# Optimization experiments

Measured on AMD Instinct MI355X. Metric: run time of the kernel, lower is better.

Reference implementation:

```python
import jax, jax.numpy as jnp
import numpy as np

EPS = 1e-6  # matches the ~1e-6 diagonal jitter added in tensor_log


def _make_spd(key, shape_bm, d):
    a = jax.random.normal(key, shape_bm + (d, d), dtype=jnp.float32)
    x = jnp.einsum('bmik,bmjk->bmij', a, a) / d
    return x + 0.1 * jnp.eye(d, dtype=jnp.float32)


def _make_stiefel(key, out_dim, in_dim):
    a = jax.random.normal(key, (in_dim, out_dim), dtype=jnp.float32)
    q, _ = jnp.linalg.qr(a)  # (in_dim, out_dim), orthonormal columns
    return q.T  # (out_dim, in_dim), semi-orthogonal rows


def setup_inputs() -> dict:
    key = jax.random.key(0)
    ks = jax.random.split(key, 8)
    bs, m, din, dqk, dv = 32, 64, 96, 48, 48
    return {
        'x1': _make_spd(ks[0], (bs, m), din),
        'x2': _make_spd(ks[1], (bs, m), din),
        'wq1': _make_stiefel(ks[2], dqk, din),
        'wk1': _make_stiefel(ks[3], dqk, din),
        'wv1': _make_stiefel(ks[4], dv, din),
        'wq2': _make_stiefel(ks[5], dqk, din),
        'wk2': _make_stiefel(ks[6], dqk, din),
        'wv2': _make_stiefel(ks[7], dv, din),
    }


def _logm(t):
    # symmetric matrix log via eigh (inputs SPD); tiny diag jitter as in torch tensor_log
    d = t.shape[-1]
    t = t + EPS * jnp.eye(d, dtype=t.dtype)
    s, u = jnp.linalg.eigh(t)
    return jnp.einsum('...ik,...k,...jk->...ij', u, jnp.log(s), u)


def _expm(t):
    s, u = jnp.linalg.eigh(t)
    return jnp.einsum('...ik,...k,...jk->...ij', u, jnp.exp(s), u)


def _bimap(x, w):
    # SPDTransform: W X W^T, W: (out, in), x: [..., in, in]
    return jnp.einsum('oi,...ij,pj->...op', w, x, w)


def reference(x1, x2, wq1, wk1, wv1, wq2, wk2, wv2):
    # per-stream q/k/v BiMap transforms, then concat along token axis
    Q = jnp.concatenate([_bimap(x1, wq1), _bimap(x2, wq2)], axis=1)  # [b, m, dqk, dqk]
    K = jnp.concatenate([_bimap(x1, wk1), _bimap(x2, wk2)], axis=1)
    V = jnp.concatenate([_bimap(x1, wv1), _bimap(x2, wv2)], axis=1)  # [b, m, dv, dv]

    logQ, logK, logV = _logm(Q), _logm(K), _logm(V)

    # log-Euclidean distance: sum of singular values of D D^T = ||D||_F^2,
    # D = logQ_j - logK_i. energy[b, i, j] matches torch repeat/expand layout
    q2 = jnp.sum(logQ * logQ, axis=(-2, -1))  # [b, m]
    k2 = jnp.sum(logK * logK, axis=(-2, -1))  # [b, m]
    cross = jnp.einsum('bjxy,bixy->bij', logQ, logK)  # [b, i(K), j(Q)]
    energy = q2[:, None, :] + k2[:, :, None] - 2.0 * cross
    energy = jnp.maximum(energy, 0.0)

    scores = 1.0 / (1.0 + jnp.log1p(energy))
    prob = jax.nn.softmax(scores, axis=-2)  # softmax over K index
    prob = jnp.transpose(prob, (0, 2, 1))   # [b, j, i]

    bs, m, dv, _ = V.shape
    mixed = (prob @ logV.reshape(bs, m, dv * dv)).reshape(bs, m, dv, dv)
    out = _expm(mixed)
    out = out[:, -1:, :, :]  # keep_only_last=True
    return out.reshape(-1, dv, dv)  # [bs, dv, dv]
```

## Files before the change

### kernel.cpp

```cpp
#include <hip/hip_runtime.h>
#include <math.h>

#define D_CHEB 24

typedef __attribute__((ext_vector_type(8))) short bf16x8;
typedef __attribute__((ext_vector_type(4))) float f32x4;
typedef __attribute__((ext_vector_type(4))) unsigned int u32x4;

struct Cheb {
    float c[D_CHEB + 1];
    float sm;
    float sbd;
};

__device__ __forceinline__ void split8(const f32x4 a, const f32x4 b,
                                       bf16x8& hi, bf16x8& lo)
{
    float v[8] = {a[0], a[1], a[2], a[3], b[0], b[1], b[2], b[3]};
    unsigned h16[8], l16[8];
    #pragma unroll
    for (int j = 0; j < 8; ++j) {
        unsigned u = __float_as_uint(v[j]);
        unsigned r = (u + 0x7FFFu + ((u >> 16) & 1u)) >> 16;
        h16[j] = r;
        float res = v[j] - __uint_as_float(r << 16);
        l16[j] = __float_as_uint(res) >> 16;
    }
    unsigned hw[4], lw[4];
    #pragma unroll
    for (int q = 0; q < 4; ++q) {
        hw[q] = h16[2 * q] | (h16[2 * q + 1] << 16);
        lw[q] = l16[2 * q] | (l16[2 * q + 1] << 16);
    }
    hi = __builtin_bit_cast(bf16x8, (u32x4){hw[0], hw[1], hw[2], hw[3]});
    lo = __builtin_bit_cast(bf16x8, (u32x4){lw[0], lw[1], lw[2], lw[3]});
}

__global__ __launch_bounds__(256) void split_w(
    const float* __restrict__ w0, const float* __restrict__ w1,
    const float* __restrict__ w2, const float* __restrict__ w3,
    const float* __restrict__ w4,
    unsigned short* __restrict__ whi, unsigned short* __restrict__ wlo)
{
    const float* W = (blockIdx.x == 0) ? w0 : (blockIdx.x == 1) ? w1
                   : (blockIdx.x == 2) ? w2 : (blockIdx.x == 3) ? w3 : w4;
    const int base = blockIdx.x * 4608;
    for (int e = threadIdx.x; e < 4608; e += 256) {
        float f = W[e];
        unsigned u = __float_as_uint(f);
        unsigned r = (u + 0x7FFFu + ((u >> 16) & 1u)) >> 16;
        whi[base + e] = (unsigned short)r;
        float res = f - __uint_as_float(r << 16);
        wlo[base + e] = (unsigned short)(__float_as_uint(res) >> 16);
    }
}

#define TLP 104
__global__ __launch_bounds__(64, 3) void bimap_kernel(
    const float* __restrict__ x1, const float* __restrict__ x2,
    const unsigned short* __restrict__ whi,
    const unsigned short* __restrict__ wlo,
    float* __restrict__ mats)
{
    __shared__ float Tlds[48 * TLP];
    const int bid = blockIdx.x, l = threadIdx.x;
    const int lc = l & 15, lg = l >> 4;

    const float* x; int wi[2]; size_t oo[2]; int npass;
    if (bid < 4096) {
        int b = bid >> 7, s = (bid >> 6) & 1, m = bid & 63;
        x = (s ? x2 : x1) + (size_t)(b * 64 + m) * 9216;
        wi[0] = s ? 2 : 0;
        wi[1] = s ? 3 : 1;
        oo[0] = (size_t)bid; oo[1] = (size_t)(4096 + bid); npass = 2;
    } else {
        int b = bid - 4096;
        x = x2 + (size_t)(b * 64 + 63) * 9216;
        wi[0] = 4; wi[1] = 4;
        oo[0] = (size_t)(8192 + b); oo[1] = oo[0]; npass = 1;
    }

    for (int pass = 0; pass < npass; ++pass) {
        const unsigned short* Wh = whi + wi[pass] * 4608;
        const unsigned short* Wl = wlo + wi[pass] * 4608;

        f32x4 C[3][6];
        #pragma unroll
        for (int tr = 0; tr < 3; ++tr)
            #pragma unroll
            for (int tc = 0; tc < 6; ++tc)
                C[tr][tc] = (f32x4){0.f, 0.f, 0.f, 0.f};
        #pragma unroll
        for (int kb = 0; kb < 3; ++kb) {
            bf16x8 ah[3], al[3];
            #pragma unroll
            for (int tr = 0; tr < 3; ++tr) {
                const int off = (16 * tr + lc) * 96 + kb * 32 + lg * 8;
                ah[tr] = *(const bf16x8*)(Wh + off);
                al[tr] = *(const bf16x8*)(Wl + off);
            }
            #pragma unroll
            for (int tc = 0; tc < 6; ++tc) {
                const float* xp = x + (16 * tc + lc) * 96 + kb * 32 + lg * 8;
                bf16x8 bh, bl;
                split8(*(const f32x4*)xp, *(const f32x4*)(xp + 4), bh, bl);
                #pragma unroll
                for (int tr = 0; tr < 3; ++tr) {
                    C[tr][tc] = __builtin_amdgcn_mfma_f32_16x16x32_bf16(ah[tr], bh, C[tr][tc], 0, 0, 0);
                    C[tr][tc] = __builtin_amdgcn_mfma_f32_16x16x32_bf16(ah[tr], bl, C[tr][tc], 0, 0, 0);
                    C[tr][tc] = __builtin_amdgcn_mfma_f32_16x16x32_bf16(al[tr], bh, C[tr][tc], 0, 0, 0);
                }
            }
        }
        #pragma unroll
        for (int tr = 0; tr < 3; ++tr)
            #pragma unroll
            for (int tc = 0; tc < 6; ++tc)
                #pragma unroll
                for (int q = 0; q < 4; ++q)
                    Tlds[(16 * tr + 4 * lg + q) * TLP + 16 * tc + lc] = C[tr][tc][q];

        f32x4 D[3][3];
        #pragma unroll
        for (int tr = 0; tr < 3; ++tr)
            #pragma unroll
            for (int tc = 0; tc < 3; ++tc)
                D[tr][tc] = (f32x4){0.f, 0.f, 0.f, 0.f};
        #pragma unroll
        for (int kb = 0; kb < 3; ++kb) {
            bf16x8 ah[3], al[3];
            #pragma unroll
            for (int tr = 0; tr < 3; ++tr) {
                const float* tp = &Tlds[(16 * tr + lc) * TLP + kb * 32 + lg * 8];
                split8(*(const f32x4*)tp, *(const f32x4*)(tp + 4), ah[tr], al[tr]);
            }
            #pragma unroll
            for (int tc = 0; tc < 3; ++tc) {
                const int off = (16 * tc + lc) * 96 + kb * 32 + lg * 8;
                bf16x8 bh = *(const bf16x8*)(Wh + off);
                bf16x8 bl = *(const bf16x8*)(Wl + off);
                #pragma unroll
                for (int tr = 0; tr < 3; ++tr) {
                    D[tr][tc] = __builtin_amdgcn_mfma_f32_16x16x32_bf16(ah[tr], bh, D[tr][tc], 0, 0, 0);
                    D[tr][tc] = __builtin_amdgcn_mfma_f32_16x16x32_bf16(ah[tr], bl, D[tr][tc], 0, 0, 0);
                    D[tr][tc] = __builtin_amdgcn_mfma_f32_16x16x32_bf16(al[tr], bh, D[tr][tc], 0, 0, 0);
                }
            }
        }
        float* out = mats + oo[pass] * 2304;
        #pragma unroll
        for (int tr = 0; tr < 3; ++tr)
            #pragma unroll
            for (int tc = 0; tc < 3; ++tc)
                #pragma unroll
                for (int q = 0; q < 4; ++q)
                    out[(16 * tr + 4 * lg + q) * 48 + 16 * tc + lc] = D[tr][tc][q];
    }
}

__global__ __launch_bounds__(64, 3) void logm_kernel(float* __restrict__ mats, Cheb co)
{
    __shared__ __align__(16) unsigned short Ybuf[2 * 48 * 64];
    char* ldsb = (char*)Ybuf;
    const int l = threadIdx.x;
    const int lc = l & 15, lg = l >> 4;
    const int rloc = lg * 4;
    float* A = mats + (size_t)blockIdx.x * 2304;

    bf16x8 Ah[3][2], Al[3][2];
    const float cD = co.c[D_CHEB], cD1 = co.c[D_CHEB - 1];
    #pragma unroll
    for (int tr = 0; tr < 3; ++tr) {
        #pragma unroll
        for (int kb = 0; kb < 2; ++kb) {
            const int row = 16 * tr + lc;
            const int k0 = kb * 32 + lg * 8;
            unsigned shw[4] = {0,0,0,0}, slw[4] = {0,0,0,0};
            unsigned yhw[4] = {0,0,0,0}, ylw[4] = {0,0,0,0};
            if (k0 < 48) {
                const float* ap = A + row * 48 + k0;
                f32x4 a0 = *(const f32x4*)ap;
                f32x4 a1 = *(const f32x4*)(ap + 4);
                float av[8] = {a0[0],a0[1],a0[2],a0[3],a1[0],a1[1],a1[2],a1[3]};
                unsigned sh[8], sl[8], yh[8], yl[8];
                #pragma unroll
                for (int j = 0; j < 8; ++j) {
                    const bool diag = (row == k0 + j);
                    float s = co.sm * av[j] + (diag ? co.sbd : 0.f);
                    float y = cD * s + (diag ? cD1 : 0.f);
                    unsigned us = __float_as_uint(s);
                    sh[j] = us >> 16;
                    sl[j] = __float_as_uint(s - __uint_as_float(us & 0xFFFF0000u)) >> 16;
                    unsigned uy = __float_as_uint(y);
                    yh[j] = uy >> 16;
                    yl[j] = __float_as_uint(y - __uint_as_float(uy & 0xFFFF0000u)) >> 16;
                }
                #pragma unroll
                for (int q = 0; q < 4; ++q) {
                    shw[q] = sh[2*q] | (sh[2*q+1] << 16);
                    slw[q] = sl[2*q] | (sl[2*q+1] << 16);
                    yhw[q] = yh[2*q] | (yh[2*q+1] << 16);
                    ylw[q] = yl[2*q] | (yl[2*q+1] << 16);
                }
            }
            Ah[tr][kb] = __builtin_bit_cast(bf16x8, (u32x4){shw[0],shw[1],shw[2],shw[3]});
            Al[tr][kb] = __builtin_bit_cast(bf16x8, (u32x4){slw[0],slw[1],slw[2],slw[3]});
            const int soff = row * 128 + ((2 * k0) ^ ((row & 7) << 4));
            *(u32x4*)(ldsb + soff)        = (u32x4){yhw[0],yhw[1],yhw[2],yhw[3]};
            *(u32x4*)(ldsb + 6144 + soff) = (u32x4){ylw[0],ylw[1],ylw[2],ylw[3]};
        }
    }

    f32x4 Ya[9], Yb[9];
    #pragma unroll
    for (int t = 0; t < 9; ++t) {
        const int tr = t / 3, tc = t % 3;
        #pragma unroll
        for (int q = 0; q < 4; ++q) {
            const int row = 16 * tr + rloc + q, col = 16 * tc + lc;
            const bool diag = (row == col);
            float a = A[row * 48 + col];
            float s = co.sm * a + (diag ? co.sbd : 0.f);
            Ya[t][q] = cD * s + (diag ? cD1 : 0.f);
            Yb[t][q] = diag ? cD : 0.f;
        }
    }

    int boff[3][2];
    #pragma unroll
    for (int tc = 0; tc < 3; ++tc)
        #pragma unroll
        for (int kb = 0; kb < 2; ++kb) {
            const int row = 16 * tc + lc;
            boff[tc][kb] = row * 128 + ((kb * 64 + lg * 16) ^ ((row & 7) << 4));
        }
    int woff[3][4];
    #pragma unroll
    for (int tc = 0; tc < 3; ++tc)
        #pragma unroll
        for (int q = 0; q < 4; ++q) {
            const int rq = rloc + q;
            woff[tc][q] = rq * 128 + ((32 * tc + 2 * lc) ^ ((rq & 7) << 4));
        }

    auto MM = [&](f32x4 (&T)[9]) {
        #pragma unroll
        for (int tc = 0; tc < 3; ++tc) {
            #pragma unroll
            for (int kb = 0; kb < 2; ++kb) {
                bf16x8 bh = *(const bf16x8*)(ldsb + boff[tc][kb]);
                bf16x8 bl = *(const bf16x8*)(ldsb + 6144 + boff[tc][kb]);
                #pragma unroll
                for (int tr = 0; tr < 3; ++tr) {
                    T[tr*3+tc] = __builtin_amdgcn_mfma_f32_16x16x32_bf16(Ah[tr][kb], bh, T[tr*3+tc], 0, 0, 0);
                    T[tr*3+tc] = __builtin_amdgcn_mfma_f32_16x16x32_bf16(Ah[tr][kb], bl, T[tr*3+tc], 0, 0, 0);
                    T[tr*3+tc] = __builtin_amdgcn_mfma_f32_16x16x32_bf16(Al[tr][kb], bh, T[tr*3+tc], 0, 0, 0);
                }
            }
        }
    };
    auto SPLITW = [&](f32x4 (&T)[9]) {
        #pragma unroll
        for (int t = 0; t < 9; ++t) {
            const int tr = t / 3, tc = t % 3;
            #pragma unroll
            for (int q = 0; q < 4; ++q) {
                float v = T[t][q];
                unsigned u = __float_as_uint(v);
                unsigned lo = __float_as_uint(v - __uint_as_float(u & 0xFFFF0000u)) >> 16;
                const int off = tr * 2048 + woff[tc][q];
                *(unsigned short*)(ldsb + off) = (unsigned short)(u >> 16);
                *(unsigned short*)(ldsb + 6144 + off) = (unsigned short)lo;
            }
        }
    };
    auto INITK = [&](f32x4 (&T)[9], float ck) {
        #pragma unroll
        for (int t = 0; t < 9; ++t) {
            const int tr = t / 3, tc = t % 3;
            #pragma unroll
            for (int q = 0; q < 4; ++q) {
                const float d = (tr == tc && rloc + q == lc) ? ck : 0.f;
                T[t][q] = d - T[t][q];
            }
        }
    };

    for (int k = D_CHEB - 2; k >= 2; k -= 2) {
        INITK(Yb, co.c[k]);     MM(Yb);  SPLITW(Yb);
        INITK(Ya, co.c[k - 1]); MM(Ya);  SPLITW(Ya);
    }
    #pragma unroll
    for (int t = 0; t < 9; ++t) {
        const int tr = t / 3, tc = t % 3;
        #pragma unroll
        for (int q = 0; q < 4; ++q) {
            const float d = (tr == tc && rloc + q == lc) ? co.c[0] : 0.f;
            Yb[t][q] = d - 2.f * Yb[t][q];
        }
    }
    MM(Yb);
    #pragma unroll
    for (int t = 0; t < 9; ++t) {
        const int tr = t / 3, tc = t % 3;
        #pragma unroll
        for (int q = 0; q < 4; ++q)
            A[(16 * tr + rloc + q) * 48 + 16 * tc + lc] = Yb[t][q];
    }
}

__global__ __launch_bounds__(64) void energy_kernel(const float* __restrict__ mats,
                                                    float* __restrict__ sc)
{
    const int i = blockIdx.x, b = blockIdx.y, lane = threadIdx.x;
    const float* K = mats + (size_t)(b * 128 + i) * 2304;
    const float* Q = mats + (size_t)(8192 + b) * 2304;
    float p = 0.f;
    #pragma unroll
    for (int j = 0; j < 9; ++j) {
        int f = (lane + 64 * j) * 4;
        float4 kv = *(const float4*)(K + f);
        float4 qv = *(const float4*)(Q + f);
        float dx = kv.x - qv.x, dy = kv.y - qv.y, dz = kv.z - qv.z, dw = kv.w - qv.w;
        p += dx * dx + dy * dy + dz * dz + dw * dw;
    }
    #pragma unroll
    for (int off = 32; off >= 1; off >>= 1) p += __shfl_xor(p, off, 64);
    if (lane == 0)
        sc[b * 128 + i] = 1.f / (1.f + log1pf(fmaxf(p, 0.f)));
}

__global__ __launch_bounds__(64) void softmax_kernel(float* __restrict__ sc)
{
    const int b = blockIdx.x, lane = threadIdx.x;
    float s0 = sc[b * 128 + lane], s1 = sc[b * 128 + 64 + lane];
    float m = fmaxf(s0, s1);
    #pragma unroll
    for (int off = 32; off >= 1; off >>= 1) m = fmaxf(m, __shfl_xor(m, off, 64));
    float e0 = expf(s0 - m), e1 = expf(s1 - m);
    float sum = e0 + e1;
    #pragma unroll
    for (int off = 32; off >= 1; off >>= 1) sum += __shfl_xor(sum, off, 64);
    sc[b * 128 + lane] = e0 / sum;
    sc[b * 128 + 64 + lane] = e1 / sum;
}

__global__ __launch_bounds__(256) void mix_kernel(const float* __restrict__ mats,
                                                  const float* __restrict__ sc,
                                                  float* __restrict__ mixed)
{
    __shared__ float w[128];
    const int b = blockIdx.y, g = blockIdx.x, tid = threadIdx.x;
    if (tid < 128) w[tid] = sc[b * 128 + tid];
    __syncthreads();
    const int e = g * 256 + tid;
    float acc = 0.f;
    for (int i = 0; i < 128; ++i)
        acc += w[i] * mats[(size_t)(4096 + b * 128 + i) * 2304 + e];
    mixed[(size_t)b * 2304 + e] = acc;
}

__global__ __launch_bounds__(256) void expm_kernel(const float* __restrict__ mixed,
                                                   float* __restrict__ out)
{
    __shared__ float Bs[48][49];
    __shared__ float Ra[48][49];
    __shared__ float Rb[48][49];
    const int b = blockIdx.x, tid = threadIdx.x;
    const float* M = mixed + (size_t)b * 2304;
    for (int e = tid; e < 2304; e += 256) {
        int r = e / 48, c = e % 48;
        float v = 0.25f * M[e];
        Bs[r][c] = v;
        Ra[r][c] = ((r == c) ? 1.f : 0.f) + v * (1.f / 12.f);
    }
    __syncthreads();
    const int tr = tid >> 4, tc = tid & 15;
    const int r0 = tr * 3, c0 = tc * 3;
    float* cur = &Ra[0][0];
    float* nxt = &Rb[0][0];
    for (int k = 11; k >= 1; --k) {
        const float invk = 1.f / (float)k;
        float acc[3][3];
        #pragma unroll
        for (int i = 0; i < 3; ++i)
            #pragma unroll
            for (int j = 0; j < 3; ++j) acc[i][j] = 0.f;
        #pragma unroll 4
        for (int kk = 0; kk < 48; ++kk) {
            float a0 = Bs[r0][kk], a1 = Bs[r0 + 1][kk], a2 = Bs[r0 + 2][kk];
            float b0 = cur[kk * 49 + c0], b1 = cur[kk * 49 + c0 + 1], b2 = cur[kk * 49 + c0 + 2];
            acc[0][0] += a0 * b0; acc[0][1] += a0 * b1; acc[0][2] += a0 * b2;
            acc[1][0] += a1 * b0; acc[1][1] += a1 * b1; acc[1][2] += a1 * b2;
            acc[2][0] += a2 * b0; acc[2][1] += a2 * b1; acc[2][2] += a2 * b2;
        }
        #pragma unroll
        for (int i = 0; i < 3; ++i)
            #pragma unroll
            for (int j = 0; j < 3; ++j)
                nxt[(r0 + i) * 49 + (c0 + j)] =
                    ((r0 + i) == (c0 + j) ? 1.f : 0.f) + acc[i][j] * invk;
        __syncthreads();
        float* t = cur; cur = nxt; nxt = t;
    }
    for (int sq = 0; sq < 2; ++sq) {
        float acc[3][3];
        #pragma unroll
        for (int i = 0; i < 3; ++i)
            #pragma unroll
            for (int j = 0; j < 3; ++j) acc[i][j] = 0.f;
        #pragma unroll 4
        for (int kk = 0; kk < 48; ++kk) {
            float a0 = cur[(r0) * 49 + kk], a1 = cur[(r0 + 1) * 49 + kk], a2 = cur[(r0 + 2) * 49 + kk];
            float b0 = cur[kk * 49 + c0], b1 = cur[kk * 49 + c0 + 1], b2 = cur[kk * 49 + c0 + 2];
            acc[0][0] += a0 * b0; acc[0][1] += a0 * b1; acc[0][2] += a0 * b2;
            acc[1][0] += a1 * b0; acc[1][1] += a1 * b1; acc[1][2] += a1 * b2;
            acc[2][0] += a2 * b0; acc[2][1] += a2 * b1; acc[2][2] += a2 * b2;
        }
        __syncthreads();
        #pragma unroll
        for (int i = 0; i < 3; ++i)
            #pragma unroll
            for (int j = 0; j < 3; ++j) nxt[(r0 + i) * 49 + (c0 + j)] = acc[i][j];
        __syncthreads();
        float* t = cur; cur = nxt; nxt = t;
    }
    #pragma unroll
    for (int i = 0; i < 3; ++i)
        #pragma unroll
        for (int j = 0; j < 3; ++j)
            out[(size_t)b * 2304 + (r0 + i) * 48 + (c0 + j)] = cur[(r0 + i) * 49 + (c0 + j)];
}

extern "C" void kernel_launch(void* const* d_in, const int* in_sizes, int n_in,
                              void* d_out, int out_size, void* d_ws, size_t ws_size,
                              hipStream_t stream)
{
    (void)in_sizes; (void)n_in; (void)out_size; (void)ws_size;
    const float* x1  = (const float*)d_in[0];
    const float* x2  = (const float*)d_in[1];
    const float* wk1 = (const float*)d_in[3];
    const float* wv1 = (const float*)d_in[4];
    const float* wq2 = (const float*)d_in[5];
    const float* wk2 = (const float*)d_in[6];
    const float* wv2 = (const float*)d_in[7];
    float* mats  = (float*)d_ws;
    float* mixed = mats + (size_t)8224 * 2304;
    float* scbuf = mixed + (size_t)32 * 2304;
    unsigned short* whi = (unsigned short*)(scbuf + 4096);
    unsigned short* wlo = whi + 5 * 4608;
    float* out   = (float*)d_out;

    Cheb co;
    {
        const double a = 0.098, bb = 5.5;
        const int N = 256;
        for (int k = 0; k <= D_CHEB; ++k) {
            double sacc = 0.0;
            for (int j = 0; j < N; ++j) {
                double th = M_PI * (j + 0.5) / N;
                double xj = 0.5 * (a + bb) + 0.5 * (bb - a) * cos(th);
                sacc += log(xj) * cos(k * th);
            }
            double ck = 2.0 * sacc / N;
            if (k == 0) ck *= 0.5;
            if (k >= 1) ck *= 0.5;
            co.c[k] = (float)ck;
        }
        co.sm  = (float)(4.0 / (bb - a));
        co.sbd = (float)((4.0 * 1e-6 - 2.0 * (a + bb)) / (bb - a));
    }

    split_w<<<5, 256, 0, stream>>>(wk1, wv1, wk2, wv2, wq2, whi, wlo);
    bimap_kernel<<<4128, 64, 0, stream>>>(x1, x2, whi, wlo, mats);
    logm_kernel<<<8224, 64, 0, stream>>>(mats, co);
    energy_kernel<<<dim3(128, 32), 64, 0, stream>>>(mats, scbuf);
    softmax_kernel<<<32, 64, 0, stream>>>(scbuf);
    mix_kernel<<<dim3(9, 32), 256, 0, stream>>>(mats, scbuf, mixed);
    expm_kernel<<<32, 256, 0, stream>>>(mixed, out);
}
```

Before: 436.5 us.

## Use 16x16x16 MFMA for K tail and store transposed packed splits

The 48-wide inner dimension is no longer padded to 64: the tail K=32..47 uses 16x16x16 bf16 MFMAs instead of a padded 16x16x32 block, which cuts wasted matrix work per Clenshaw step. The hi/lo split writeback now stores the result transposed as packed 64-bit LDS writes instead of per-element 16-bit stores, reducing LDS store instructions. This relies on the matrix being symmetric for the transposed layout to be valid and adds a compile-time fallback path.

```diff
diff --git a/kernel.cpp b/kernel.cpp
--- a/kernel.cpp
+++ b/kernel.cpp
@@ -4,8 +4,16 @@
 #define D_CHEB 24
 
 typedef __attribute__((ext_vector_type(8))) short bf16x8;
+typedef __attribute__((ext_vector_type(4))) short bf16x4;
 typedef __attribute__((ext_vector_type(4))) float f32x4;
 typedef __attribute__((ext_vector_type(4))) unsigned int u32x4;
+typedef __attribute__((ext_vector_type(2))) unsigned int u32x2;
+
+#if __has_builtin(__builtin_amdgcn_mfma_f32_16x16x16bf16_1k)
+#define HAVE_MFMA16 1
+#else
+#define HAVE_MFMA16 0
+#endif
 
 struct Cheb {
     float c[D_CHEB + 1];
@@ -211,6 +219,27 @@
         }
     }
 
+#if HAVE_MFMA16
+    bf16x4 Ath[3], Atl[3];
+    #pragma unroll
+    for (int tr = 0; tr < 3; ++tr) {
+        const int row = 16 * tr + lc;
+        const int k0 = 32 + 4 * lg;
+        f32x4 a = *(const f32x4*)(A + row * 48 + k0);
+        unsigned sh[4], sl[4];
+        #pragma unroll
+        for (int j = 0; j < 4; ++j) {
+            const bool diag = (row == k0 + j);
+            float s = co.sm * a[j] + (diag ? co.sbd : 0.f);
+            unsigned us = __float_as_uint(s);
+            sh[j] = us >> 16;
+            sl[j] = __float_as_uint(s - __uint_as_float(us & 0xFFFF0000u)) >> 16;
+        }
+        Ath[tr] = __builtin_bit_cast(bf16x4, (u32x2){sh[0] | (sh[1] << 16), sh[2] | (sh[3] << 16)});
+        Atl[tr] = __builtin_bit_cast(bf16x4, (u32x2){sl[0] | (sl[1] << 16), sl[2] | (sl[3] << 16)});
+    }
+#endif
+
     f32x4 Ya[9], Yb[9];
     #pragma unroll
     for (int t = 0; t < 9; ++t) {
@@ -226,52 +255,90 @@
         }
     }
 
-    int boff[3][2];
-    #pragma unroll
-    for (int tc = 0; tc < 3; ++tc)
-        #pragma unroll
-        for (int kb = 0; kb < 2; ++kb) {
-            const int row = 16 * tc + lc;
-            boff[tc][kb] = row * 128 + ((kb * 64 + lg * 16) ^ ((row & 7) << 4));
-        }
-    int woff[3][4];
-    #pragma unroll
-    for (int tc = 0; tc < 3; ++tc)
-        #pragma unroll
-        for (int q = 0; q < 4; ++q) {
-            const int rq = rloc + q;
-            woff[tc][q] = rq * 128 + ((32 * tc + 2 * lc) ^ ((rq & 7) << 4));
-        }
+    int boff0[3];
+    int bofft[3];
+    int boff1[3];
+    #pragma unroll
+    for (int tc = 0; tc < 3; ++tc) {
+        const int row = 16 * tc + lc;
+        const int sw = (row & 7) << 4;
+        boff0[tc] = row * 128 + ((lg * 16) ^ sw);
+        bofft[tc] = row * 128 + ((64 + lg * 8) ^ sw);
+        boff1[tc] = row * 128 + ((64 + lg * 16) ^ sw);
+    }
+    int woffT[9];
+    #pragma unroll
+    for (int t = 0; t < 9; ++t) {
+        const int tr = t / 3, tc = t % 3;
+        const int row = 16 * tc + lc;
+        woffT[t] = row * 128 + (((32 * tr + 8 * lg)) ^ ((row & 7) << 4));
+    }
 
     auto MM = [&](f32x4 (&T)[9]) {
         #pragma unroll
         for (int tc = 0; tc < 3; ++tc) {
-            #pragma unroll
-            for (int kb = 0; kb < 2; ++kb) {
-                bf16x8 bh = *(const bf16x8*)(ldsb + boff[tc][kb]);
-                bf16x8 bl = *(const bf16x8*)(ldsb + 6144 + boff[tc][kb]);
-                #pragma unroll
-                for (int tr = 0; tr < 3; ++tr) {
-                    T[tr*3+tc] = __builtin_amdgcn_mfma_f32_16x16x32_bf16(Ah[tr][kb], bh, T[tr*3+tc], 0, 0, 0);
-                    T[tr*3+tc] = __builtin_amdgcn_mfma_f32_16x16x32_bf16(Ah[tr][kb], bl, T[tr*3+tc], 0, 0, 0);
-                    T[tr*3+tc] = __builtin_amdgcn_mfma_f32_16x16x32_bf16(Al[tr][kb], bh, T[tr*3+tc], 0, 0, 0);
-                }
-            }
+            {
+                bf16x8 bh = *(const bf16x8*)(ldsb + boff0[tc]);
+                bf16x8 bl = *(const bf16x8*)(ldsb + 6144 + boff0[tc]);
+                #pragma unroll
+                for (int tr = 0; tr < 3; ++tr)
+                    T[tr*3+tc] = __builtin_amdgcn_mfma_f32_16x16x32_bf16(Ah[tr][0], bh, T[tr*3+tc], 0, 0, 0);
+                #pragma unroll
+                for (int tr = 0; tr < 3; ++tr)
+                    T[tr*3+tc] = __builtin_amdgcn_mfma_f32_16x16x32_bf16(Ah[tr][0], bl, T[tr*3+tc], 0, 0, 0);
+                #pragma unroll
+                for (int tr = 0; tr < 3; ++tr)
+                    T[tr*3+tc] = __builtin_amdgcn_mfma_f32_16x16x32_bf16(Al[tr][0], bh, T[tr*3+tc], 0, 0, 0);
+            }
+#if HAVE_MFMA16
+            {
+                bf16x4 bh = *(const bf16x4*)(ldsb + bofft[tc]);
+                bf16x4 bl = *(const bf16x4*)(ldsb + 6144 + bofft[tc]);
+                #pragma unroll
+                for (int tr = 0; tr < 3; ++tr)
+                    T[tr*3+tc] = __builtin_amdgcn_mfma_f32_16x16x16bf16_1k(Ath[tr], bh, T[tr*3+tc], 0, 0, 0);
+                #pragma unroll
+                for (int tr = 0; tr < 3; ++tr)
+                    T[tr*3+tc] = __builtin_amdgcn_mfma_f32_16x16x16bf16_1k(Ath[tr], bl, T[tr*3+tc], 0, 0, 0);
+                #pragma unroll
+                for (int tr = 0; tr < 3; ++tr)
+                    T[tr*3+tc] = __builtin_amdgcn_mfma_f32_16x16x16bf16_1k(Atl[tr], bh, T[tr*3+tc], 0, 0, 0);
+            }
+#else
+            {
+                bf16x8 bh = *(const bf16x8*)(ldsb + boff1[tc]);
+                bf16x8 bl = *(const bf16x8*)(ldsb + 6144 + boff1[tc]);
+                #pragma unroll
+                for (int tr = 0; tr < 3; ++tr)
+                    T[tr*3+tc] = __builtin_amdgcn_mfma_f32_16x16x32_bf16(Ah[tr][1], bh, T[tr*3+tc], 0, 0, 0);
+                #pragma unroll
+                for (int tr = 0; tr < 3; ++tr)
+                    T[tr*3+tc] = __builtin_amdgcn_mfma_f32_16x16x32_bf16(Ah[tr][1], bl, T[tr*3+tc], 0, 0, 0);
+                #pragma unroll
+                for (int tr = 0; tr < 3; ++tr)
+                    T[tr*3+tc] = __builtin_amdgcn_mfma_f32_16x16x32_bf16(Al[tr][1], bh, T[tr*3+tc], 0, 0, 0);
+            }
+#endif
         }
     };
-    auto SPLITW = [&](f32x4 (&T)[9]) {
+    auto SPLITWT = [&](f32x4 (&T)[9]) {
         #pragma unroll
         for (int t = 0; t < 9; ++t) {
-            const int tr = t / 3, tc = t % 3;
-            #pragma unroll
-            for (int q = 0; q < 4; ++q) {
-                float v = T[t][q];
-                unsigned u = __float_as_uint(v);
-                unsigned lo = __float_as_uint(v - __uint_as_float(u & 0xFFFF0000u)) >> 16;
-                const int off = tr * 2048 + woff[tc][q];
-                *(unsigned short*)(ldsb + off) = (unsigned short)(u >> 16);
-                *(unsigned short*)(ldsb + 6144 + off) = (unsigned short)lo;
-            }
+            unsigned u0 = __float_as_uint(T[t][0]);
+            unsigned u1 = __float_as_uint(T[t][1]);
+            unsigned u2 = __float_as_uint(T[t][2]);
+            unsigned u3 = __float_as_uint(T[t][3]);
+            unsigned h01 = (u1 & 0xFFFF0000u) | (u0 >> 16);
+            unsigned h23 = (u3 & 0xFFFF0000u) | (u2 >> 16);
+            float r0 = T[t][0] - __uint_as_float(u0 & 0xFFFF0000u);
+            float r1 = T[t][1] - __uint_as_float(u1 & 0xFFFF0000u);
+            float r2 = T[t][2] - __uint_as_float(u2 & 0xFFFF0000u);
+            float r3 = T[t][3] - __uint_as_float(u3 & 0xFFFF0000u);
+            unsigned l01 = (__float_as_uint(r1) & 0xFFFF0000u) | (__float_as_uint(r0) >> 16);
+            unsigned l23 = (__float_as_uint(r3) & 0xFFFF0000u) | (__float_as_uint(r2) >> 16);
+            const int off = woffT[t];
+            *(u32x2*)(ldsb + off)        = (u32x2){h01, h23};
+            *(u32x2*)(ldsb + 6144 + off) = (u32x2){l01, l23};
         }
     };
     auto INITK = [&](f32x4 (&T)[9], float ck) {
@@ -287,8 +354,8 @@
     };
 
     for (int k = D_CHEB - 2; k >= 2; k -= 2) {
-        INITK(Yb, co.c[k]);     MM(Yb);  SPLITW(Yb);
-        INITK(Ya, co.c[k - 1]); MM(Ya);  SPLITW(Ya);
+        INITK(Yb, co.c[k]);     MM(Yb);  SPLITWT(Yb);
+        INITK(Ya, co.c[k - 1]); MM(Ya);  SPLITWT(Ya);
     }
     #pragma unroll
     for (int t = 0; t < 9; ++t) {
```

New measurement: 415.2 us. 4.9% less time.
